# Kernel optimization log

Hardware: AMD Instinct MI355X
Metric: run time of the kernel (lower is better)

The kernel has to match this reference:

```python
import jax, jax.numpy as jnp
import numpy as np

N_NODES = 6890
N_ANGLES = 8
K_CHEB = 15
N_DESC = 544
HIDDEN = 64
N_CLASS = 6890
M = N_ANGLES * N_NODES  # 55120, size of anisotropic Laplacian
DEG = 16
NNZ = M * DEG
BN_EPS = 1e-5


def setup_inputs() -> dict:
    key = jax.random.key(0)
    ks = jax.random.split(key, 16)
    x = jax.random.normal(ks[0], (N_NODES, N_DESC), dtype=jnp.float32)
    # sparse anisotropic Laplacian (M x M), ~DEG nnz per row
    rows = jnp.repeat(jnp.arange(M, dtype=jnp.int32), DEG)
    cols = jax.random.randint(ks[1], (NNZ,), 0, M, dtype=jnp.int32)
    vals = jax.random.normal(ks[2], (NNZ,), dtype=jnp.float32) * 0.1
    # conv1: (K, n_angles*n_desc, 64); conv2..6 stacked: (5, K, n_angles*64, 64)
    def xavier(k, shape, fan_in, fan_out):
        lim = np.sqrt(6.0 / (fan_in + fan_out))
        return jax.random.uniform(k, shape, jnp.float32, -lim, lim)
    W1 = xavier(ks[3], (K_CHEB, N_ANGLES * N_DESC, HIDDEN), N_ANGLES * N_DESC, HIDDEN)
    Wc = xavier(ks[4], (5, K_CHEB, N_ANGLES * HIDDEN, HIDDEN), N_ANGLES * HIDDEN, HIDDEN)
    conv_b = jnp.zeros((6, HIDDEN), jnp.float32)
    bn_gamma = jnp.ones((6, HIDDEN), jnp.float32)
    bn_beta = jnp.zeros((6, HIDDEN), jnp.float32)
    fc2_w = xavier(ks[5], (HIDDEN, 256), HIDDEN, 256)
    fc2_b = jnp.zeros((256,), jnp.float32)
    fc3_w = xavier(ks[6], (256, N_CLASS), 256, N_CLASS)
    fc3_b = jnp.zeros((N_CLASS,), jnp.float32)
    return {"x": x, "rows": rows, "cols": cols, "vals": vals,
            "W1": W1, "Wc": Wc, "conv_b": conv_b,
            "bn_gamma": bn_gamma, "bn_beta": bn_beta,
            "fc2_w": fc2_w, "fc2_b": fc2_b, "fc3_w": fc3_w, "fc3_b": fc3_b}


def _spmm(rows, cols, vals, T):
    # (M x M sparse) @ (M x C) via gather + segment-sum
    return jax.ops.segment_sum(vals[:, None] * T[cols], rows, num_segments=M)


def _acs_conv(x, rows, cols, vals, W, b):
    # x: (N, C). Chebyshev recurrence on the (A*N, C) angle-stacked signal.
    N, C = x.shape
    A = N_ANGLES

    def proj(T, Wk):
        # (A*N, C) -> (N, A*C) @ (A*C, out)
        return T.reshape(A, N, C).transpose(1, 0, 2).reshape(N, A * C) @ Wk

    T0 = jnp.tile(x, (A, 1))
    out = proj(T0, W[0])
    T1 = _spmm(rows, cols, vals, T0)
    out = out + proj(T1, W[1])
    for k in range(2, K_CHEB):
        T2 = 2.0 * _spmm(rows, cols, vals, T1) - T0
        out = out + proj(T2, W[k])
        T0, T1 = T1, T2
    return out + b


def _bn_relu(x, gamma, beta):
    # BatchNorm1d (training-mode batch stats, biased variance) + ReLU
    mean = jnp.mean(x, axis=0)
    var = jnp.var(x, axis=0)
    return jax.nn.relu((x - mean) * jax.lax.rsqrt(var + BN_EPS) * gamma + beta)


def reference(x, rows, cols, vals, W1, Wc, conv_b, bn_gamma, bn_beta,
              fc2_w, fc2_b, fc3_w, fc3_b):
    h = _bn_relu(_acs_conv(x, rows, cols, vals, W1, conv_b[0]), bn_gamma[0], bn_beta[0])
    for i in range(5):
        h = _bn_relu(_acs_conv(h, rows, cols, vals, Wc[i], conv_b[i + 1]),
                     bn_gamma[i + 1], bn_beta[i + 1])
    h = jax.nn.relu(h @ fc2_w + fc2_b)
    # dropout is identity at inference
    return h @ fc3_w + fc3_b
```

## Files before the change

### kernel.cpp

```cpp
#include <hip/hip_runtime.h>
#include <cstdint>
#include <cstddef>

#define NN 6890
#define NA 8
#define KC 15
#define ND 544
#define MR (NA * NN)
#define DEG 16
#define NNZ (MR * DEG)
#define BN_EPS 1e-5f
#define NRG 108
#define PB (NA * NRG)

typedef unsigned int u32;
typedef _Float16 f16;
typedef __attribute__((ext_vector_type(8))) _Float16 f16x8;
typedef __attribute__((ext_vector_type(4))) float f32x4;

union U4H8 { uint4 q; f16 h[8]; f16x8 v; };

__device__ __forceinline__ u32 packh(float a, float b) {
    union { f16 h[2]; u32 u; } c;
    c.h[0] = (f16)a; c.h[1] = (f16)b; return c.u;
}
__device__ __forceinline__ uint4 pack8h(const float* t) {
    uint4 m;
    m.x = packh(t[0], t[1]); m.y = packh(t[2], t[3]);
    m.z = packh(t[4], t[5]); m.w = packh(t[6], t[7]);
    return m;
}
__device__ __forceinline__ void acc8h(float* s, float v, uint4 g) {
    U4H8 c; c.q = g;
    #pragma unroll
    for (int i = 0; i < 8; ++i) s[i] += v * (float)c.h[i];
}

__global__ __launch_bounds__(256)
void prep_cv_kernel(const int* __restrict__ cols, const float* __restrict__ vals,
                    uint4* __restrict__ cvq)
{
    const int q = blockIdx.x * 256 + threadIdx.x;
    if (q >= NNZ / 4) return;
    const int4   c = ((const int4*)cols)[q];
    const float4 v = ((const float4*)vals)[q];
    uint4 o;
    o.x = ((u32)c.x & 0xffffu) | ((u32)c.y << 16);
    o.y = ((u32)c.z & 0xffffu) | ((u32)c.w << 16);
    o.z = packh(v.x, v.y);
    o.w = packh(v.z, v.w);
    cvq[q] = o;
}

template<int CC, bool BN>
__global__ __launch_bounds__(256)
void tile_slab_kernel(const float* __restrict__ X, int C_in, int c0,
                      uint4* __restrict__ slab0, const float* __restrict__ bnp)
{
    constexpr int LPR = CC / 8;
    constexpr int RPB = 256 / LPR;
    const int tid = threadIdx.x;
    const int j = tid % LPR, rloc = tid / LPR;
    const int r = blockIdx.x * RPB + rloc;
    if (r >= MR) return;
    const int n = r % NN;
    const float* xp = X + (size_t)n * C_in + c0 + 8 * j;
    const float4 t0 = *(const float4*)xp;
    const float4 t1 = *(const float4*)(xp + 4);
    float t[8] = { t0.x, t0.y, t0.z, t0.w, t1.x, t1.y, t1.z, t1.w };
    if (BN) {
        const int ch = c0 + 8 * j;
        #pragma unroll
        for (int i = 0; i < 8; ++i) {
            const float v = t[i] * bnp[ch + i] + bnp[64 + ch + i];
            t[i] = v > 0.f ? v : 0.f;
        }
    }
    slab0[(size_t)r * LPR + j] = pack8h(t);
}

template<int CC, bool CHEB>
__device__ __forceinline__
void spmm_body(const uint4* __restrict__ sp, const uint4* __restrict__ sc,
               uint4* __restrict__ sw, const uint4* __restrict__ cvq,
               uint4* cvl)
{
    constexpr int LPR = CC / 8;
    constexpr int RPB = 256 / LPR;
    const int tid = threadIdx.x;
    const int j = tid % LPR, rloc = tid / LPR;
    const int r0 = blockIdx.x * RPB;
    const int nrow = (MR - r0) < RPB ? (MR - r0) : RPB;
    for (int e = tid; e < nrow * 4; e += 256)
        cvl[e] = cvq[(size_t)r0 * 4 + e];
    __syncthreads();
    const int r = r0 + rloc;
    if (r >= MR) return;

    int c[16]; float v[16];
    #pragma unroll
    for (int q = 0; q < 4; ++q) {
        const uint4 cq = cvl[rloc * 4 + q];
        c[4 * q + 0] = cq.x & 0xffffu; c[4 * q + 1] = cq.x >> 16;
        c[4 * q + 2] = cq.y & 0xffffu; c[4 * q + 3] = cq.y >> 16;
        union { u32 u; f16 h[2]; } z, w_;
        z.u = cq.z; w_.u = cq.w;
        v[4 * q + 0] = (float)z.h[0]; v[4 * q + 1] = (float)z.h[1];
        v[4 * q + 2] = (float)w_.h[0]; v[4 * q + 3] = (float)w_.h[1];
    }
    float s[8] = {0.f, 0.f, 0.f, 0.f, 0.f, 0.f, 0.f, 0.f};
    #pragma unroll
    for (int d = 0; d < DEG; ++d)
        acc8h(s, v[d], sp[(size_t)c[d] * LPR + j]);
    float t[8];
    if (CHEB) {
        U4H8 p; p.q = sc[(size_t)r * LPR + j];
        #pragma unroll
        for (int i = 0; i < 8; ++i) t[i] = 2.f * s[i] - (float)p.h[i];
    } else {
        #pragma unroll
        for (int i = 0; i < 8; ++i) t[i] = s[i];
    }
    sw[(size_t)r * LPR + j] = pack8h(t);
}

template<int CC, bool CHEB>
__global__ __launch_bounds__(256)
void spmm_only_kernel(const uint4* __restrict__ sp, const uint4* __restrict__ sc,
                      uint4* __restrict__ sw, const uint4* __restrict__ cvq)
{
    constexpr int RPB = 256 / (CC / 8);
    __shared__ uint4 cvl[RPB * 4];
    spmm_body<CC, CHEB>(sp, sc, sw, cvq, cvl);
}

template<int SCC, int NPROJ, bool FIRSTP>
__device__ __forceinline__
void proj_body(int pb, const uint4* __restrict__ s0, const uint4* __restrict__ s1,
               const float* __restrict__ W, float* __restrict__ part,
               int C_in, int c0, int kbase, u32* WH, u32* WL)
{
    constexpr int LPRF   = SCC / 8;
    constexpr int SLICES = SCC >= 64 ? SCC / 64 : 1;
    constexpr int SCH    = SCC >= 64 ? 64 : SCC;
    constexpr int CCH    = SCH / 32;
    const int tid = threadIdx.x;
    const int l = tid & 63, w = tid >> 6;
    const int a = pb / NRG, rg = pb % NRG;
    const int rows0 = rg * 64;
    const int hi16 = l >> 4;

    const int arow = rows0 + w * 16 + (l & 15);
    const int arc  = arow < NN ? arow : NN - 1;
    const size_t abase = (size_t)(a * NN + arc) * LPRF;

    f32x4 acc[4];
    #pragma unroll
    for (int nt = 0; nt < 4; ++nt) {
        #pragma unroll
        for (int rr = 0; rr < 4; ++rr) {
            const int orow = rows0 + w * 16 + hi16 * 4 + rr;
            float vv = 0.f;
            if (!FIRSTP && orow < NN)
                vv = part[((size_t)a * NN + orow) * 64 + nt * 16 + (l & 15)];
            acc[nt][rr] = vv;
        }
    }

    #pragma unroll
    for (int p = 0; p < NPROJ; ++p) {
        const uint4* sl = (p == 0) ? s0 : s1;
        #pragma unroll
        for (int s = 0; s < SLICES; ++s) {
            const float* Wk = W + ((size_t)(kbase + p) * NA * C_in
                                   + (size_t)a * C_in + c0 + s * 64) * 64;
            if (p | s) __syncthreads();
            for (int e = tid; e < CCH * 1024; e += 256) {
                const int i2 = e & 3;
                const int ll = (e >> 2) & 63;
                const int nt = (e >> 8) & 3;
                const int h  = e >> 10;
                const int cc  = h * 32 + (ll >> 4) * 8 + 2 * i2;
                const int col = nt * 16 + (ll & 15);
                const float w0 = Wk[(size_t)cc * 64 + col];
                const float w1 = Wk[(size_t)(cc + 1) * 64 + col];
                const f16 h0 = (f16)w0, h1 = (f16)w1;
                union { f16 h[2]; u32 u; } ph, pl;
                ph.h[0] = h0; ph.h[1] = h1;
                pl.h[0] = (f16)(w0 - (float)h0); pl.h[1] = (f16)(w1 - (float)h1);
                WH[e] = ph.u; WL[e] = pl.u;
            }
            __syncthreads();
            #pragma unroll
            for (int h = 0; h < CCH; ++h) {
                U4H8 af; af.q = sl[abase + s * 8 + h * 4 + hi16];
                #pragma unroll
                for (int nt = 0; nt < 4; ++nt) {
                    const int be = ((h * 4 + nt) * 64 + l) * 4;
                    U4H8 bh, bl;
                    bh.q = *(const uint4*)&WH[be];
                    bl.q = *(const uint4*)&WL[be];
                    acc[nt] = __builtin_amdgcn_mfma_f32_16x16x32_f16(af.v, bh.v, acc[nt], 0, 0, 0);
                    acc[nt] = __builtin_amdgcn_mfma_f32_16x16x32_f16(af.v, bl.v, acc[nt], 0, 0, 0);
                }
            }
        }
    }

    #pragma unroll
    for (int nt = 0; nt < 4; ++nt) {
        #pragma unroll
        for (int rr = 0; rr < 4; ++rr) {
            const int orow = rows0 + w * 16 + hi16 * 4 + rr;
            if (orow < NN)
                part[((size_t)a * NN + orow) * 64 + nt * 16 + (l & 15)] = acc[nt][rr];
        }
    }
}

template<int CC, bool FIRSTP>
__global__ __launch_bounds__(256)
void step2_kernel(const uint4* __restrict__ sp, const uint4* __restrict__ sc,
                  uint4* __restrict__ sw, const uint4* __restrict__ cvq,
                  const float* __restrict__ W, float* __restrict__ part,
                  int C_in, int c0, int kbase, int NB)
{
    constexpr int RPB = 256 / (CC / 8);
    __shared__ uint4 cvl[RPB * 4];
    __shared__ u32 WH[2048];
    __shared__ u32 WL[2048];
    if ((int)blockIdx.x < NB)
        spmm_body<CC, true>(sp, sc, sw, cvq, cvl);
    else
        proj_body<CC, 2, FIRSTP>((int)blockIdx.x - NB, sc, sp, W, part, C_in, c0, kbase, WH, WL);
}

template<int CC>
__global__ __launch_bounds__(256)
void proj_final_kernel(const uint4* __restrict__ sl, const float* __restrict__ W,
                       float* __restrict__ part, int C_in, int c0, int kproj)
{
    __shared__ u32 WH[2048];
    __shared__ u32 WL[2048];
    proj_body<CC, 1, false>((int)blockIdx.x, sl, sl, W, part, C_in, c0, kproj, WH, WL);
}

__global__ void bn_reduce_kernel(const float* __restrict__ part, float* __restrict__ acc)
{
    const int e = blockIdx.x * blockDim.x + threadIdx.x;
    if (e >= NN * 64) return;
    float s = 0.f;
    #pragma unroll
    for (int a = 0; a < NA; ++a) s += part[(size_t)a * NN * 64 + e];
    acc[e] = s;
}

__global__ __launch_bounds__(256)
void bn_stats_kernel(const float* __restrict__ acc, const float* __restrict__ gamma,
                     const float* __restrict__ beta, float* __restrict__ bnp)
{
    const int h = blockIdx.x;
    float s = 0.f, sq = 0.f;
    for (int n = threadIdx.x; n < NN; n += 256) {
        const float v = acc[(size_t)n * 64 + h];
        s += v; sq += v * v;
    }
    __shared__ float ls[256], lq[256];
    ls[threadIdx.x] = s; lq[threadIdx.x] = sq;
    __syncthreads();
    for (int st = 128; st > 0; st >>= 1) {
        if (threadIdx.x < st) { ls[threadIdx.x] += ls[threadIdx.x + st]; lq[threadIdx.x] += lq[threadIdx.x + st]; }
        __syncthreads();
    }
    if (threadIdx.x == 0) {
        const float mean = ls[0] / (float)NN;
        const float var  = lq[0] / (float)NN - mean * mean;
        const float sc   = gamma[h] / sqrtf(var + BN_EPS);
        bnp[h]      = sc;
        bnp[64 + h] = beta[h] - mean * sc;
    }
}

__global__ void bn_apply_kernel(const float* __restrict__ acc, const float* __restrict__ bnp,
                                float* __restrict__ H)
{
    const int e = blockIdx.x * blockDim.x + threadIdx.x;
    if (e >= NN * 64) return;
    const int h = e & 63;
    const float v = acc[e] * bnp[h] + bnp[64 + h];
    H[e] = v > 0.f ? v : 0.f;
}

template<bool RELU>
__global__ __launch_bounds__(256)
void gemm_bias_kernel(const float* __restrict__ A, const float* __restrict__ B,
                      const float* __restrict__ bias, float* __restrict__ C,
                      int Mm, int Nn, int Kk)
{
    __shared__ float As[16][132];
    __shared__ float Bs[16][132];
    const int tx = threadIdx.x & 15, ty = threadIdx.x >> 4;
    const int m0 = blockIdx.y * 128, n0 = blockIdx.x * 128;
    const bool full = (m0 + 128 <= Mm) && (n0 + 128 <= Nn);
    float acc[8][8] = {};
    for (int k0 = 0; k0 < Kk; k0 += 16) {
        if (full) {
            #pragma unroll
            for (int e = threadIdx.x; e < 512; e += 256) {
                const int i = e >> 2, q = e & 3;
                const float4 a4 = *(const float4*)&A[(size_t)(m0 + i) * Kk + k0 + 4 * q];
                As[4 * q + 0][i] = a4.x; As[4 * q + 1][i] = a4.y;
                As[4 * q + 2][i] = a4.z; As[4 * q + 3][i] = a4.w;
            }
            #pragma unroll
            for (int e = threadIdx.x; e < 512; e += 256) {
                const int kk = e >> 5, q = e & 31;
                *(float4*)&Bs[kk][4 * q] = *(const float4*)&B[(size_t)(k0 + kk) * Nn + n0 + 4 * q];
            }
        } else {
            for (int e = threadIdx.x; e < 128 * 16; e += 256) {
                const int i = e >> 4, kk = e & 15;
                const int row = m0 + i;
                As[kk][i] = (row < Mm) ? A[(size_t)row * Kk + k0 + kk] : 0.f;
            }
            for (int e = threadIdx.x; e < 16 * 128; e += 256) {
                const int kk = e >> 7, jj = e & 127;
                const int col = n0 + jj;
                Bs[kk][jj] = (col < Nn) ? B[(size_t)(k0 + kk) * Nn + col] : 0.f;
            }
        }
        __syncthreads();
        #pragma unroll
        for (int kk = 0; kk < 16; ++kk) {
            float av[8], bv[8];
            *(float4*)&av[0] = *(const float4*)&As[kk][ty * 4];
            *(float4*)&av[4] = *(const float4*)&As[kk][64 + ty * 4];
            *(float4*)&bv[0] = *(const float4*)&Bs[kk][tx * 4];
            *(float4*)&bv[4] = *(const float4*)&Bs[kk][64 + tx * 4];
            #pragma unroll
            for (int i = 0; i < 8; ++i)
                #pragma unroll
                for (int jj = 0; jj < 8; ++jj)
                    acc[i][jj] += av[i] * bv[jj];
        }
        __syncthreads();
    }
    for (int i = 0; i < 8; ++i) {
        const int row = m0 + (i < 4 ? ty * 4 + i : 64 + ty * 4 + (i - 4));
        if (row >= Mm) continue;
        for (int jj = 0; jj < 8; ++jj) {
            const int col = n0 + (jj < 4 ? tx * 4 + jj : 64 + tx * 4 + (jj - 4));
            if (col >= Nn) continue;
            float v = acc[i][jj] + bias[col];
            if (RELU) v = fmaxf(v, 0.f);
            C[(size_t)row * Nn + col] = v;
        }
    }
}

__global__ __launch_bounds__(256)
void w3_split_kernel(const float* __restrict__ W, f16* __restrict__ Wh, f16* __restrict__ Wl)
{
    __shared__ float t[64][65];
    const int tid = threadIdx.x;
    const int n0 = blockIdx.x * 64, k0 = blockIdx.y * 64;
    for (int e = tid; e < 64 * 64; e += 256) {
        const int kk = e >> 6, nn = e & 63;
        const int gn = n0 + nn;
        t[kk][nn] = (gn < NN) ? W[(size_t)(k0 + kk) * NN + gn] : 0.f;
    }
    __syncthreads();
    for (int e = tid; e < 64 * 8; e += 256) {
        const int nn = e >> 3, c8 = e & 7;
        const int gn = n0 + nn;
        if (gn >= NN) continue;
        const size_t ob = ((size_t)((k0 >> 3) + c8) * NN + gn) * 8;
        f16 vh[8], vl[8];
        #pragma unroll
        for (int i = 0; i < 8; ++i) {
            const float w = t[c8 * 8 + i][nn];
            const f16 h = (f16)w;
            vh[i] = h; vl[i] = (f16)(w - (float)h);
        }
        *(uint4*)&Wh[ob] = *(const uint4*)vh;
        *(uint4*)&Wl[ob] = *(const uint4*)vl;
    }
}

__global__ __launch_bounds__(256)
void f2_split_kernel(const float* __restrict__ f2, f16* __restrict__ Ah, f16* __restrict__ Al)
{
    const int row = blockIdx.x * 256 + threadIdx.x;
    const int c = blockIdx.y;
    if (row >= NN) return;
    const float4 a0 = *(const float4*)&f2[(size_t)row * 256 + c * 8];
    const float4 a1 = *(const float4*)&f2[(size_t)row * 256 + c * 8 + 4];
    const float vv[8] = { a0.x, a0.y, a0.z, a0.w, a1.x, a1.y, a1.z, a1.w };
    f16 vh[8], vl[8];
    #pragma unroll
    for (int i = 0; i < 8; ++i) {
        const f16 h = (f16)vv[i];
        vh[i] = h; vl[i] = (f16)(vv[i] - (float)h);
    }
    const size_t ob = ((size_t)c * NN + row) * 8;
    *(uint4*)&Ah[ob] = *(const uint4*)vh;
    *(uint4*)&Al[ob] = *(const uint4*)vl;
}

__global__ __launch_bounds__(256)
void fc3_mfma_kernel(const f16* __restrict__ Ah, const f16* __restrict__ Al,
                     const f16* __restrict__ Bh, const f16* __restrict__ Bl,
                     const float* __restrict__ bias, float* __restrict__ C)
{
    const int tid = threadIdx.x, l = tid & 63, w = tid >> 6;
    const int wm = w >> 1, wn = w & 1, hi16 = l >> 4;
    const int m0 = blockIdx.y * 128, n0 = blockIdx.x * 128;

    size_t aoff[4], boff[4];
    #pragma unroll
    for (int mf = 0; mf < 4; ++mf) {
        int row = m0 + wm * 64 + mf * 16 + (l & 15);
        if (row > NN - 1) row = NN - 1;
        aoff[mf] = (size_t)row * 8;
    }
    #pragma unroll
    for (int nf = 0; nf < 4; ++nf) {
        int col = n0 + wn * 64 + nf * 16 + (l & 15);
        if (col > NN - 1) col = NN - 1;
        boff[nf] = (size_t)col * 8;
    }

    f32x4 acc[4][4];
    #pragma unroll
    for (int mf = 0; mf < 4; ++mf)
        #pragma unroll
        for (int nf = 0; nf < 4; ++nf)
            acc[mf][nf] = (f32x4){0.f, 0.f, 0.f, 0.f};

    for (int k0 = 0; k0 < 256; k0 += 32) {
        const size_t cb = (size_t)((k0 >> 3) + hi16) * NN * 8;
        f16x8 ah[4], al[4], bh[4], bl[4];
        #pragma unroll
        for (int mf = 0; mf < 4; ++mf) {
            ah[mf] = *(const f16x8*)(Ah + cb + aoff[mf]);
            al[mf] = *(const f16x8*)(Al + cb + aoff[mf]);
        }
        #pragma unroll
        for (int nf = 0; nf < 4; ++nf) {
            bh[nf] = *(const f16x8*)(Bh + cb + boff[nf]);
            bl[nf] = *(const f16x8*)(Bl + cb + boff[nf]);
        }
        #pragma unroll
        for (int mf = 0; mf < 4; ++mf)
            #pragma unroll
            for (int nf = 0; nf < 4; ++nf) {
                acc[mf][nf] = __builtin_amdgcn_mfma_f32_16x16x32_f16(ah[mf], bh[nf], acc[mf][nf], 0, 0, 0);
                acc[mf][nf] = __builtin_amdgcn_mfma_f32_16x16x32_f16(ah[mf], bl[nf], acc[mf][nf], 0, 0, 0);
                acc[mf][nf] = __builtin_amdgcn_mfma_f32_16x16x32_f16(al[mf], bh[nf], acc[mf][nf], 0, 0, 0);
            }
    }

    #pragma unroll
    for (int mf = 0; mf < 4; ++mf) {
        #pragma unroll
        for (int nf = 0; nf < 4; ++nf) {
            const int col = n0 + wn * 64 + nf * 16 + (l & 15);
            if (col >= NN) continue;
            const float bv = bias[col];
            #pragma unroll
            for (int rr = 0; rr < 4; ++rr) {
                const int row = m0 + wm * 64 + mf * 16 + hi16 * 4 + rr;
                if (row < NN)
                    C[(size_t)row * NN + col] = acc[mf][nf][rr] + bv;
            }
        }
    }
}

template<int CC, bool BN>
static void run_chunk(bool first, const float* X, int C_in, int c0,
                      const uint4* cvq, const float* W, const float* bnp,
                      uint4* slabs, float* part, hipStream_t stream)
{
    constexpr int RPB = 256 / (CC / 8);
    const int NB = (MR + RPB - 1) / RPB;
    const size_t SLOT = (size_t)MR * (CC / 8);
    uint4* sl[3] = { slabs, slabs + SLOT, slabs + 2 * SLOT };

    tile_slab_kernel<CC, BN><<<NB, 256, 0, stream>>>(X, C_in, c0, sl[0], bnp);
    spmm_only_kernel<CC, false><<<NB, 256, 0, stream>>>(sl[0], sl[0], sl[1], cvq);
    for (int k = 2; k < KC; ++k) {
        const int p = (k - 1) % 3, c = (k - 2) % 3, n = k % 3;
        if (k & 1) {
            spmm_only_kernel<CC, true><<<NB, 256, 0, stream>>>(sl[p], sl[c], sl[n], cvq);
        } else {
            if (first && k == 2)
                step2_kernel<CC, true ><<<NB + PB, 256, 0, stream>>>(
                    sl[p], sl[c], sl[n], cvq, W, part, C_in, c0, k - 2, NB);
            else
                step2_kernel<CC, false><<<NB + PB, 256, 0, stream>>>(
                    sl[p], sl[c], sl[n], cvq, W, part, C_in, c0, k - 2, NB);
        }
    }
    proj_final_kernel<CC><<<PB, 256, 0, stream>>>(sl[(KC - 1) % 3], W, part, C_in, c0, KC - 1);
}

extern "C" void kernel_launch(void* const* d_in, const int* in_sizes, int n_in,
                              void* d_out, int out_size, void* d_ws, size_t ws_size,
                              hipStream_t stream)
{
    (void)in_sizes; (void)n_in; (void)out_size; (void)ws_size;
    const float* x     = (const float*)d_in[0];
    const int*   cols  = (const int*)  d_in[2];
    const float* vals  = (const float*)d_in[3];
    const float* W1    = (const float*)d_in[4];
    const float* Wc    = (const float*)d_in[5];
    const float* gamma = (const float*)d_in[7];
    const float* beta  = (const float*)d_in[8];
    const float* fc2w  = (const float*)d_in[9];
    const float* fc2b  = (const float*)d_in[10];
    const float* fc3w  = (const float*)d_in[11];
    const float* fc3b  = (const float*)d_in[12];

    const size_t MT = (size_t)MR * 64;

    uint4* slabs = (uint4*)d_out;

    char* base = (char*)d_ws;
    size_t off = 0;
    uint4* cvq  = (uint4*)(base + off); off += (size_t)(NNZ / 4) * 16;
    float* part = (float*)(base + off); off += MT * 4;
    float* acc  = (float*)(base + off); off += (size_t)NN * 64 * 4;
    float* H    = (float*)(base + off); off += (size_t)NN * 64 * 4;
    float* f2   = (float*)(base + off); off += (size_t)NN * 256 * 4;
    f16* f2h    = (f16*)(base + off);   off += (size_t)NN * 256 * 2;
    f16* f2l    = (f16*)(base + off);   off += (size_t)NN * 256 * 2;
    f16* W3h    = (f16*)(base + off);   off += (size_t)NN * 256 * 2;
    f16* W3l    = (f16*)(base + off);   off += (size_t)NN * 256 * 2;
    float* bnp  = (float*)(base + off);

    prep_cv_kernel<<<(NNZ / 4 + 255) / 256, 256, 0, stream>>>(cols, vals, cvq);
    w3_split_kernel<<<dim3(108, 4), 256, 0, stream>>>(fc3w, W3h, W3l);

    for (int li = 0; li < 6; ++li) {
        const int C_in = (li == 0) ? ND : 64;
        const float* W = (li == 0) ? W1 : Wc + (size_t)(li - 1) * KC * (NA * 64) * 64;

        if (li == 0) {
            run_chunk<256, false>(true,  x, C_in, 0,   cvq, W, nullptr, slabs, part, stream);
            run_chunk<256, false>(false, x, C_in, 256, cvq, W, nullptr, slabs, part, stream);
            run_chunk<32,  false>(false, x, C_in, 512, cvq, W, nullptr, slabs, part, stream);
        } else {
            run_chunk<64, true>(true, acc, C_in, 0, cvq, W, bnp, slabs, part, stream);
        }

        bn_reduce_kernel<<<(NN * 64 + 255) / 256, 256, 0, stream>>>(part, acc);
        bn_stats_kernel<<<64, 256, 0, stream>>>(acc, gamma + li * 64, beta + li * 64, bnp);
        if (li == 5)
            bn_apply_kernel<<<(NN * 64 + 255) / 256, 256, 0, stream>>>(acc, bnp, H);
    }

    gemm_bias_kernel<true><<<dim3(2, 54), 256, 0, stream>>>(H, fc2w, fc2b, f2, NN, 256, 64);
    f2_split_kernel<<<dim3(27, 32), 256, 0, stream>>>(f2, f2h, f2l);
    fc3_mfma_kernel<<<dim3(54, 54), 256, 0, stream>>>(f2h, f2l, W3h, W3l, fc3b, (float*)d_out);
}
```

Before: 4.085 ms.

## Batch layer-0 chunks into joint launches, batch projections, fuse fc2 split, remap fc3 tiles

Layer 0 previously ran three chunk pipelines one after another. They now run in single combined launches for tiling, SpMM and SpMM+projection, with separate ring buffers so the chunks proceed together. Hidden layers use a 5-slot ring so each projection pass handles four Chebyshev terms at once, which cuts the read-modify-write traffic on the partial accumulator. fc2 now writes the f16 hi/lo split directly, removing a kernel and an fp32 buffer, and fc3 uses an XCD-aware tile remap for better L2 locality. In exchange it needs more workspace and more complex kernels.

New measurement: 3.876 ms. 5.1% less time.

```diff
diff --git a/kernel.cpp b/kernel.cpp
--- a/kernel.cpp
+++ b/kernel.cpp
@@ -12,13 +12,19 @@
 #define BN_EPS 1e-5f
 #define NRG 108
 #define PB (NA * NRG)
+#define NB256 6890
+#define NB32  862
+#define NB64  1723
 
 typedef unsigned int u32;
 typedef _Float16 f16;
 typedef __attribute__((ext_vector_type(8))) _Float16 f16x8;
+typedef __attribute__((ext_vector_type(4))) _Float16 f16x4;
 typedef __attribute__((ext_vector_type(4))) float f32x4;
 
 union U4H8 { uint4 q; f16 h[8]; f16x8 v; };
+
+struct Slabs4 { const uint4* s[4]; };
 
 __device__ __forceinline__ u32 packh(float a, float b) {
     union { f16 h[2]; u32 u; } c;
@@ -53,15 +59,15 @@
 }
 
 template<int CC, bool BN>
-__global__ __launch_bounds__(256)
-void tile_slab_kernel(const float* __restrict__ X, int C_in, int c0,
-                      uint4* __restrict__ slab0, const float* __restrict__ bnp)
+__device__ __forceinline__
+void tile_body(int bid, const float* __restrict__ X, int C_in, int c0,
+               uint4* __restrict__ slab0, const float* __restrict__ bnp)
 {
     constexpr int LPR = CC / 8;
     constexpr int RPB = 256 / LPR;
     const int tid = threadIdx.x;
     const int j = tid % LPR, rloc = tid / LPR;
-    const int r = blockIdx.x * RPB + rloc;
+    const int r = bid * RPB + rloc;
     if (r >= MR) return;
     const int n = r % NN;
     const float* xp = X + (size_t)n * C_in + c0 + 8 * j;
@@ -79,17 +85,34 @@
     slab0[(size_t)r * LPR + j] = pack8h(t);
 }
 
+__global__ __launch_bounds__(256)
+void tile_l0_kernel(const float* __restrict__ X,
+                    uint4* __restrict__ sA, uint4* __restrict__ sB,
+                    uint4* __restrict__ sT)
+{
+    const int bid = blockIdx.x;
+    if (bid < NB256)            tile_body<256, false>(bid, X, ND, 0, sA, nullptr);
+    else if (bid < 2 * NB256)   tile_body<256, false>(bid - NB256, X, ND, 256, sB, nullptr);
+    else                        tile_body<32,  false>(bid - 2 * NB256, X, ND, 512, sT, nullptr);
+}
+
+__global__ __launch_bounds__(256)
+void tile64_bn_kernel(const float* __restrict__ X, uint4* __restrict__ slab0,
+                      const float* __restrict__ bnp)
+{
+    tile_body<64, true>(blockIdx.x, X, 64, 0, slab0, bnp);
+}
+
 template<int CC, bool CHEB>
 __device__ __forceinline__
-void spmm_body(const uint4* __restrict__ sp, const uint4* __restrict__ sc,
-               uint4* __restrict__ sw, const uint4* __restrict__ cvq,
-               uint4* cvl)
+void spmm_body(int bid, const uint4* __restrict__ sp, const uint4* __restrict__ sc,
+               uint4* __restrict__ sw, const uint4* __restrict__ cvq, uint4* cvl)
 {
     constexpr int LPR = CC / 8;
     constexpr int RPB = 256 / LPR;
     const int tid = threadIdx.x;
     const int j = tid % LPR, rloc = tid / LPR;
-    const int r0 = blockIdx.x * RPB;
+    const int r0 = bid * RPB;
     const int nrow = (MR - r0) < RPB ? (MR - r0) : RPB;
     for (int e = tid; e < nrow * 4; e += 256)
         cvl[e] = cvq[(size_t)r0 * 4 + e];
@@ -124,39 +147,14 @@
     sw[(size_t)r * LPR + j] = pack8h(t);
 }
 
-template<int CC, bool CHEB>
-__global__ __launch_bounds__(256)
-void spmm_only_kernel(const uint4* __restrict__ sp, const uint4* __restrict__ sc,
-                      uint4* __restrict__ sw, const uint4* __restrict__ cvq)
-{
-    constexpr int RPB = 256 / (CC / 8);
-    __shared__ uint4 cvl[RPB * 4];
-    spmm_body<CC, CHEB>(sp, sc, sw, cvq, cvl);
-}
-
-template<int SCC, int NPROJ, bool FIRSTP>
+template<bool FIRSTP>
 __device__ __forceinline__
-void proj_body(int pb, const uint4* __restrict__ s0, const uint4* __restrict__ s1,
-               const float* __restrict__ W, float* __restrict__ part,
-               int C_in, int c0, int kbase, u32* WH, u32* WL)
-{
-    constexpr int LPRF   = SCC / 8;
-    constexpr int SLICES = SCC >= 64 ? SCC / 64 : 1;
-    constexpr int SCH    = SCC >= 64 ? 64 : SCC;
-    constexpr int CCH    = SCH / 32;
-    const int tid = threadIdx.x;
-    const int l = tid & 63, w = tid >> 6;
-    const int a = pb / NRG, rg = pb % NRG;
-    const int rows0 = rg * 64;
+void proj_ld(f32x4 (&acc)[4], const float* __restrict__ part, int a, int rows0,
+             int l, int w)
+{
     const int hi16 = l >> 4;
-
-    const int arow = rows0 + w * 16 + (l & 15);
-    const int arc  = arow < NN ? arow : NN - 1;
-    const size_t abase = (size_t)(a * NN + arc) * LPRF;
-
-    f32x4 acc[4];
-    #pragma unroll
-    for (int nt = 0; nt < 4; ++nt) {
+    #pragma unroll
+    for (int nt = 0; nt < 4; ++nt)
         #pragma unroll
         for (int rr = 0; rr < 4; ++rr) {
             const int orow = rows0 + w * 16 + hi16 * 4 + rr;
@@ -165,16 +163,48 @@
                 vv = part[((size_t)a * NN + orow) * 64 + nt * 16 + (l & 15)];
             acc[nt][rr] = vv;
         }
-    }
+}
+
+__device__ __forceinline__
+void proj_st(const f32x4 (&acc)[4], float* __restrict__ part, int a, int rows0,
+             int l, int w)
+{
+    const int hi16 = l >> 4;
+    #pragma unroll
+    for (int nt = 0; nt < 4; ++nt)
+        #pragma unroll
+        for (int rr = 0; rr < 4; ++rr) {
+            const int orow = rows0 + w * 16 + hi16 * 4 + rr;
+            if (orow < NN)
+                part[((size_t)a * NN + orow) * 64 + nt * 16 + (l & 15)] = acc[nt][rr];
+        }
+}
+
+template<int SCC, int NPROJ>
+__device__ __forceinline__
+void proj_accum(int a, int rows0, int l, int w, Slabs4 sl,
+                const float* __restrict__ W, int C_in, int c0, int kbase,
+                u32* WH, u32* WL, f32x4 (&acc)[4], bool presync)
+{
+    constexpr int LPRF   = SCC / 8;
+    constexpr int SLICES = SCC >= 64 ? SCC / 64 : 1;
+    constexpr int SCH    = SCC >= 64 ? 64 : SCC;
+    constexpr int CCH    = SCH / 32;
+    const int tid = threadIdx.x;
+    const int hi16 = l >> 4;
+    const int arow = rows0 + w * 16 + (l & 15);
+    const int arc  = arow < NN ? arow : NN - 1;
+    const size_t abase = (size_t)(a * NN + arc) * LPRF;
 
     #pragma unroll
     for (int p = 0; p < NPROJ; ++p) {
-        const uint4* sl = (p == 0) ? s0 : s1;
+        const uint4* slab = sl.s[p];
         #pragma unroll
         for (int s = 0; s < SLICES; ++s) {
             const float* Wk = W + ((size_t)(kbase + p) * NA * C_in
                                    + (size_t)a * C_in + c0 + s * 64) * 64;
             if (p | s) __syncthreads();
+            else if (presync) __syncthreads();
             for (int e = tid; e < CCH * 1024; e += 256) {
                 const int i2 = e & 3;
                 const int ll = (e >> 2) & 63;
@@ -193,7 +223,7 @@
             __syncthreads();
             #pragma unroll
             for (int h = 0; h < CCH; ++h) {
-                U4H8 af; af.q = sl[abase + s * 8 + h * 4 + hi16];
+                U4H8 af; af.q = slab[abase + s * 8 + h * 4 + hi16];
                 #pragma unroll
                 for (int nt = 0; nt < 4; ++nt) {
                     const int be = ((h * 4 + nt) * 64 + l) * 4;
@@ -206,43 +236,115 @@
             }
         }
     }
-
-    #pragma unroll
-    for (int nt = 0; nt < 4; ++nt) {
-        #pragma unroll
-        for (int rr = 0; rr < 4; ++rr) {
-            const int orow = rows0 + w * 16 + hi16 * 4 + rr;
-            if (orow < NN)
-                part[((size_t)a * NN + orow) * 64 + nt * 16 + (l & 15)] = acc[nt][rr];
-        }
-    }
-}
-
-template<int CC, bool FIRSTP>
-__global__ __launch_bounds__(256)
-void step2_kernel(const uint4* __restrict__ sp, const uint4* __restrict__ sc,
-                  uint4* __restrict__ sw, const uint4* __restrict__ cvq,
-                  const float* __restrict__ W, float* __restrict__ part,
-                  int C_in, int c0, int kbase, int NB)
-{
-    constexpr int RPB = 256 / (CC / 8);
-    __shared__ uint4 cvl[RPB * 4];
+}
+
+template<bool CHEB>
+__global__ __launch_bounds__(256)
+void spmm_l0_kernel(const uint4* __restrict__ sAp, const uint4* __restrict__ sAc, uint4* __restrict__ sAw,
+                    const uint4* __restrict__ sBp, const uint4* __restrict__ sBc, uint4* __restrict__ sBw,
+                    const uint4* __restrict__ sTp, const uint4* __restrict__ sTc, uint4* __restrict__ sTw,
+                    const uint4* __restrict__ cvq)
+{
+    __shared__ uint4 cvl[256];
+    const int bid = blockIdx.x;
+    if (bid < NB256)          spmm_body<256, CHEB>(bid, sAp, sAc, sAw, cvq, cvl);
+    else if (bid < 2 * NB256) spmm_body<256, CHEB>(bid - NB256, sBp, sBc, sBw, cvq, cvl);
+    else                      spmm_body<32,  CHEB>(bid - 2 * NB256, sTp, sTc, sTw, cvq, cvl);
+}
+
+template<bool FIRSTP>
+__global__ __launch_bounds__(256)
+void step_l0_proj_kernel(const uint4* __restrict__ sAp, const uint4* __restrict__ sAc, uint4* __restrict__ sAw,
+                         const uint4* __restrict__ sBp, const uint4* __restrict__ sBc, uint4* __restrict__ sBw,
+                         const uint4* __restrict__ sTp, const uint4* __restrict__ sTc, uint4* __restrict__ sTw,
+                         const uint4* __restrict__ cvq, const float* __restrict__ W,
+                         float* __restrict__ part, int kbase)
+{
+    __shared__ uint4 cvl[256];
     __shared__ u32 WH[2048];
     __shared__ u32 WL[2048];
-    if ((int)blockIdx.x < NB)
-        spmm_body<CC, true>(sp, sc, sw, cvq, cvl);
-    else
-        proj_body<CC, 2, FIRSTP>((int)blockIdx.x - NB, sc, sp, W, part, C_in, c0, kbase, WH, WL);
-}
-
-template<int CC>
-__global__ __launch_bounds__(256)
-void proj_final_kernel(const uint4* __restrict__ sl, const float* __restrict__ W,
-                       float* __restrict__ part, int C_in, int c0, int kproj)
+    const int bid = blockIdx.x;
+    if (bid < NB256)          { spmm_body<256, true>(bid, sAp, sAc, sAw, cvq, cvl); return; }
+    if (bid < 2 * NB256)      { spmm_body<256, true>(bid - NB256, sBp, sBc, sBw, cvq, cvl); return; }
+    if (bid < 2 * NB256 + NB32) { spmm_body<32, true>(bid - 2 * NB256, sTp, sTc, sTw, cvq, cvl); return; }
+    const int pb = bid - (2 * NB256 + NB32);
+    const int l = threadIdx.x & 63, w = threadIdx.x >> 6;
+    const int a = pb / NRG, rows0 = (pb % NRG) * 64;
+    f32x4 acc[4];
+    proj_ld<FIRSTP>(acc, part, a, rows0, l, w);
+    Slabs4 sa; sa.s[0] = sAc; sa.s[1] = sAp;
+    Slabs4 sb; sb.s[0] = sBc; sb.s[1] = sBp;
+    Slabs4 st; st.s[0] = sTc; st.s[1] = sTp;
+    proj_accum<256, 2>(a, rows0, l, w, sa, W, ND, 0,   kbase, WH, WL, acc, false);
+    proj_accum<256, 2>(a, rows0, l, w, sb, W, ND, 256, kbase, WH, WL, acc, true);
+    proj_accum<32,  2>(a, rows0, l, w, st, W, ND, 512, kbase, WH, WL, acc, true);
+    proj_st(acc, part, a, rows0, l, w);
+}
+
+__global__ __launch_bounds__(256)
+void proj_l0_final_kernel(const uint4* __restrict__ sA, const uint4* __restrict__ sB,
+                          const uint4* __restrict__ sT, const float* __restrict__ W,
+                          float* __restrict__ part, int kbase)
 {
     __shared__ u32 WH[2048];
     __shared__ u32 WL[2048];
-    proj_body<CC, 1, false>((int)blockIdx.x, sl, sl, W, part, C_in, c0, kproj, WH, WL);
+    const int pb = blockIdx.x;
+    const int l = threadIdx.x & 63, w = threadIdx.x >> 6;
+    const int a = pb / NRG, rows0 = (pb % NRG) * 64;
+    f32x4 acc[4];
+    proj_ld<false>(acc, part, a, rows0, l, w);
+    Slabs4 sa; sa.s[0] = sA;
+    Slabs4 sb; sb.s[0] = sB;
+    Slabs4 st; st.s[0] = sT;
+    proj_accum<256, 1>(a, rows0, l, w, sa, W, ND, 0,   kbase, WH, WL, acc, false);
+    proj_accum<256, 1>(a, rows0, l, w, sb, W, ND, 256, kbase, WH, WL, acc, true);
+    proj_accum<32,  1>(a, rows0, l, w, st, W, ND, 512, kbase, WH, WL, acc, true);
+    proj_st(acc, part, a, rows0, l, w);
+}
+
+template<bool CHEB>
+__global__ __launch_bounds__(256)
+void spmm64_kernel(const uint4* __restrict__ sp, const uint4* __restrict__ sc,
+                   uint4* __restrict__ sw, const uint4* __restrict__ cvq)
+{
+    __shared__ uint4 cvl[128];
+    spmm_body<64, CHEB>(blockIdx.x, sp, sc, sw, cvq, cvl);
+}
+
+template<bool FIRSTP>
+__global__ __launch_bounds__(256)
+void step64_proj4_kernel(const uint4* __restrict__ sp, const uint4* __restrict__ sc,
+                         uint4* __restrict__ sw, Slabs4 prj,
+                         const uint4* __restrict__ cvq, const float* __restrict__ W,
+                         float* __restrict__ part, int kbase)
+{
+    __shared__ uint4 cvl[128];
+    __shared__ u32 WH[2048];
+    __shared__ u32 WL[2048];
+    const int bid = blockIdx.x;
+    if (bid < NB64) { spmm_body<64, true>(bid, sp, sc, sw, cvq, cvl); return; }
+    const int pb = bid - NB64;
+    const int l = threadIdx.x & 63, w = threadIdx.x >> 6;
+    const int a = pb / NRG, rows0 = (pb % NRG) * 64;
+    f32x4 acc[4];
+    proj_ld<FIRSTP>(acc, part, a, rows0, l, w);
+    proj_accum<64, 4>(a, rows0, l, w, prj, W, 64, 0, kbase, WH, WL, acc, false);
+    proj_st(acc, part, a, rows0, l, w);
+}
+
+__global__ __launch_bounds__(256)
+void proj64_final_kernel(Slabs4 prj, const float* __restrict__ W,
+                         float* __restrict__ part, int kbase)
+{
+    __shared__ u32 WH[2048];
+    __shared__ u32 WL[2048];
+    const int pb = blockIdx.x;
+    const int l = threadIdx.x & 63, w = threadIdx.x >> 6;
+    const int a = pb / NRG, rows0 = (pb % NRG) * 64;
+    f32x4 acc[4];
+    proj_ld<false>(acc, part, a, rows0, l, w);
+    proj_accum<64, 3>(a, rows0, l, w, prj, W, 64, 0, kbase, WH, WL, acc, false);
+    proj_st(acc, part, a, rows0, l, w);
 }
 
 __global__ void bn_reduce_kernel(const float* __restrict__ part, float* __restrict__ acc)
@@ -291,17 +393,17 @@
     H[e] = v > 0.f ? v : 0.f;
 }
 
-template<bool RELU>
-__global__ __launch_bounds__(256)
-void gemm_bias_kernel(const float* __restrict__ A, const float* __restrict__ B,
-                      const float* __restrict__ bias, float* __restrict__ C,
-                      int Mm, int Nn, int Kk)
-{
+__global__ __launch_bounds__(256)
+void fc2_kernel(const float* __restrict__ A, const float* __restrict__ B,
+                const float* __restrict__ bias,
+                f16* __restrict__ Oh, f16* __restrict__ Ol)
+{
+    constexpr int Kk = 64, Nn = 256;
     __shared__ float As[16][132];
     __shared__ float Bs[16][132];
     const int tx = threadIdx.x & 15, ty = threadIdx.x >> 4;
     const int m0 = blockIdx.y * 128, n0 = blockIdx.x * 128;
-    const bool full = (m0 + 128 <= Mm) && (n0 + 128 <= Nn);
+    const bool full = (m0 + 128 <= NN);
     float acc[8][8] = {};
     for (int k0 = 0; k0 < Kk; k0 += 16) {
         if (full) {
@@ -312,22 +414,17 @@
                 As[4 * q + 0][i] = a4.x; As[4 * q + 1][i] = a4.y;
                 As[4 * q + 2][i] = a4.z; As[4 * q + 3][i] = a4.w;
             }
-            #pragma unroll
-            for (int e = threadIdx.x; e < 512; e += 256) {
-                const int kk = e >> 5, q = e & 31;
-                *(float4*)&Bs[kk][4 * q] = *(const float4*)&B[(size_t)(k0 + kk) * Nn + n0 + 4 * q];
-            }
         } else {
             for (int e = threadIdx.x; e < 128 * 16; e += 256) {
                 const int i = e >> 4, kk = e & 15;
                 const int row = m0 + i;
-                As[kk][i] = (row < Mm) ? A[(size_t)row * Kk + k0 + kk] : 0.f;
-            }
-            for (int e = threadIdx.x; e < 16 * 128; e += 256) {
-                const int kk = e >> 7, jj = e & 127;
-                const int col = n0 + jj;
-                Bs[kk][jj] = (col < Nn) ? B[(size_t)(k0 + kk) * Nn + col] : 0.f;
-            }
+                As[kk][i] = (row < NN) ? A[(size_t)row * Kk + k0 + kk] : 0.f;
+            }
+        }
+        #pragma unroll
+        for (int e = threadIdx.x; e < 512; e += 256) {
+            const int kk = e >> 5, q = e & 31;
+            *(float4*)&Bs[kk][4 * q] = *(const float4*)&B[(size_t)(k0 + kk) * Nn + n0 + 4 * q];
         }
         __syncthreads();
         #pragma unroll
@@ -345,15 +442,24 @@
         }
         __syncthreads();
     }
+    #pragma unroll
     for (int i = 0; i < 8; ++i) {
         const int row = m0 + (i < 4 ? ty * 4 + i : 64 + ty * 4 + (i - 4));
-        if (row >= Mm) continue;
-        for (int jj = 0; jj < 8; ++jj) {
-            const int col = n0 + (jj < 4 ? tx * 4 + jj : 64 + tx * 4 + (jj - 4));
-            if (col >= Nn) continue;
-            float v = acc[i][jj] + bias[col];
-            if (RELU) v = fmaxf(v, 0.f);
-            C[(size_t)row * Nn + col] = v;
+        if (row >= NN) continue;
+        #pragma unroll
+        for (int g = 0; g < 2; ++g) {
+            const int colg = n0 + (g ? 64 : 0) + tx * 4;
+            f16x4 vh, vl;
+            #pragma unroll
+            for (int jj = 0; jj < 4; ++jj) {
+                float v = acc[i][g * 4 + jj] + bias[colg + jj];
+                v = fmaxf(v, 0.f);
+                const f16 h = (f16)v;
+                vh[jj] = h; vl[jj] = (f16)(v - (float)h);
+            }
+            const size_t ob = ((size_t)(colg >> 3) * NN + row) * 8 + (colg & 7);
+            *(f16x4*)&Oh[ob] = vh;
+            *(f16x4*)&Ol[ob] = vl;
         }
     }
 }
@@ -388,33 +494,19 @@
 }
 
 __global__ __launch_bounds__(256)
-void f2_split_kernel(const float* __restrict__ f2, f16* __restrict__ Ah, f16* __restrict__ Al)
-{
-    const int row = blockIdx.x * 256 + threadIdx.x;
-    const int c = blockIdx.y;
-    if (row >= NN) return;
-    const float4 a0 = *(const float4*)&f2[(size_t)row * 256 + c * 8];
-    const float4 a1 = *(const float4*)&f2[(size_t)row * 256 + c * 8 + 4];
-    const float vv[8] = { a0.x, a0.y, a0.z, a0.w, a1.x, a1.y, a1.z, a1.w };
-    f16 vh[8], vl[8];
-    #pragma unroll
-    for (int i = 0; i < 8; ++i) {
-        const f16 h = (f16)vv[i];
-        vh[i] = h; vl[i] = (f16)(vv[i] - (float)h);
-    }
-    const size_t ob = ((size_t)c * NN + row) * 8;
-    *(uint4*)&Ah[ob] = *(const uint4*)vh;
-    *(uint4*)&Al[ob] = *(const uint4*)vl;
-}
-
-__global__ __launch_bounds__(256)
 void fc3_mfma_kernel(const f16* __restrict__ Ah, const f16* __restrict__ Al,
                      const f16* __restrict__ Bh, const f16* __restrict__ Bl,
                      const float* __restrict__ bias, float* __restrict__ C)
 {
+    const int o = blockIdx.x;
+    const int xcd = o & 7, jj0 = o >> 3;
+    const int wg = (xcd < 4 ? xcd * 365 : 4 * 365 + (xcd - 4) * 364) + jj0;
+    const int band = wg / 486, inb = wg % 486;
+    const int mt = inb / 9, nt = band * 9 + inb % 9;
+    const int m0 = mt * 128, n0 = nt * 128;
+
     const int tid = threadIdx.x, l = tid & 63, w = tid >> 6;
     const int wm = w >> 1, wn = w & 1, hi16 = l >> 4;
-    const int m0 = blockIdx.y * 128, n0 = blockIdx.x * 128;
 
     size_t aoff[4], boff[4];
     #pragma unroll
@@ -475,34 +567,6 @@
             }
         }
     }
-}
-
-template<int CC, bool BN>
-static void run_chunk(bool first, const float* X, int C_in, int c0,
-                      const uint4* cvq, const float* W, const float* bnp,
-                      uint4* slabs, float* part, hipStream_t stream)
-{
-    constexpr int RPB = 256 / (CC / 8);
-    const int NB = (MR + RPB - 1) / RPB;
-    const size_t SLOT = (size_t)MR * (CC / 8);
-    uint4* sl[3] = { slabs, slabs + SLOT, slabs + 2 * SLOT };
-
-    tile_slab_kernel<CC, BN><<<NB, 256, 0, stream>>>(X, C_in, c0, sl[0], bnp);
-    spmm_only_kernel<CC, false><<<NB, 256, 0, stream>>>(sl[0], sl[0], sl[1], cvq);
-    for (int k = 2; k < KC; ++k) {
-        const int p = (k - 1) % 3, c = (k - 2) % 3, n = k % 3;
-        if (k & 1) {
-            spmm_only_kernel<CC, true><<<NB, 256, 0, stream>>>(sl[p], sl[c], sl[n], cvq);
-        } else {
-            if (first && k == 2)
-                step2_kernel<CC, true ><<<NB + PB, 256, 0, stream>>>(
-                    sl[p], sl[c], sl[n], cvq, W, part, C_in, c0, k - 2, NB);
-            else
-                step2_kernel<CC, false><<<NB + PB, 256, 0, stream>>>(
-                    sl[p], sl[c], sl[n], cvq, W, part, C_in, c0, k - 2, NB);
-        }
-    }
-    proj_final_kernel<CC><<<PB, 256, 0, stream>>>(sl[(KC - 1) % 3], W, part, C_in, c0, KC - 1);
 }
 
 extern "C" void kernel_launch(void* const* d_in, const int* in_sizes, int n_in,
@@ -524,43 +588,85 @@
 
     const size_t MT = (size_t)MR * 64;
 
-    uint4* slabs = (uint4*)d_out;
+    const size_t SL256 = (size_t)MR * 32;
+    const size_t SL32  = (size_t)MR * 4;
+    uint4* ringA = (uint4*)d_out;
+    uint4* ringB = ringA + 3 * SL256;
+    uint4* ringT = ringB + 3 * SL256;
+    auto slA = [&](int k) { return ringA + (size_t)(k % 3) * SL256; };
+    auto slB = [&](int k) { return ringB + (size_t)(k % 3) * SL256; };
+    auto slT = [&](int k) { return ringT + (size_t)(k % 3) * SL32; };
 
     char* base = (char*)d_ws;
     size_t off = 0;
     uint4* cvq  = (uint4*)(base + off); off += (size_t)(NNZ / 4) * 16;
+    uint4* ring5 = (uint4*)(base + off); off += 5 * (size_t)MR * 8 * 16;
     float* part = (float*)(base + off); off += MT * 4;
     float* acc  = (float*)(base + off); off += (size_t)NN * 64 * 4;
     float* H    = (float*)(base + off); off += (size_t)NN * 64 * 4;
-    float* f2   = (float*)(base + off); off += (size_t)NN * 256 * 4;
     f16* f2h    = (f16*)(base + off);   off += (size_t)NN * 256 * 2;
     f16* f2l    = (f16*)(base + off);   off += (size_t)NN * 256 * 2;
     f16* W3h    = (f16*)(base + off);   off += (size_t)NN * 256 * 2;
     f16* W3l    = (f16*)(base + off);   off += (size_t)NN * 256 * 2;
     float* bnp  = (float*)(base + off);
+    const size_t SL64 = (size_t)MR * 8;
+    auto sl5 = [&](int k) { return ring5 + (size_t)(k % 5) * SL64; };
 
     prep_cv_kernel<<<(NNZ / 4 + 255) / 256, 256, 0, stream>>>(cols, vals, cvq);
     w3_split_kernel<<<dim3(108, 4), 256, 0, stream>>>(fc3w, W3h, W3l);
 
-    for (int li = 0; li < 6; ++li) {
-        const int C_in = (li == 0) ? ND : 64;
-        const float* W = (li == 0) ? W1 : Wc + (size_t)(li - 1) * KC * (NA * 64) * 64;
-
-        if (li == 0) {
-            run_chunk<256, false>(true,  x, C_in, 0,   cvq, W, nullptr, slabs, part, stream);
-            run_chunk<256, false>(false, x, C_in, 256, cvq, W, nullptr, slabs, part, stream);
-            run_chunk<32,  false>(false, x, C_in, 512, cvq, W, nullptr, slabs, part, stream);
-        } else {
-            run_chunk<64, true>(true, acc, C_in, 0, cvq, W, bnp, slabs, part, stream);
-        }
-
+    {
+        const float* W = W1;
+        tile_l0_kernel<<<2 * NB256 + NB32, 256, 0, stream>>>(x, slA(0), slB(0), slT(0));
+        spmm_l0_kernel<false><<<2 * NB256 + NB32, 256, 0, stream>>>(
+            slA(0), slA(0), slA(1), slB(0), slB(0), slB(1), slT(0), slT(0), slT(1), cvq);
+        for (int k = 2; k < KC; ++k) {
+            if (k & 1) {
+                spmm_l0_kernel<true><<<2 * NB256 + NB32, 256, 0, stream>>>(
+                    slA(k - 1), slA(k - 2), slA(k), slB(k - 1), slB(k - 2), slB(k),
+                    slT(k - 1), slT(k - 2), slT(k), cvq);
+            } else if (k == 2) {
+                step_l0_proj_kernel<true><<<2 * NB256 + NB32 + PB, 256, 0, stream>>>(
+                    slA(k - 1), slA(k - 2), slA(k), slB(k - 1), slB(k - 2), slB(k),
+                    slT(k - 1), slT(k - 2), slT(k), cvq, W, part, k - 2);
+            } else {
+                step_l0_proj_kernel<false><<<2 * NB256 + NB32 + PB, 256, 0, stream>>>(
+                    slA(k - 1), slA(k - 2), slA(k), slB(k - 1), slB(k - 2), slB(k),
+                    slT(k - 1), slT(k - 2), slT(k), cvq, W, part, k - 2);
+            }
+        }
+        proj_l0_final_kernel<<<PB, 256, 0, stream>>>(slA(14), slB(14), slT(14), W, part, 14);
+        bn_reduce_kernel<<<(NN * 64 + 255) / 256, 256, 0, stream>>>(part, acc);
+        bn_stats_kernel<<<64, 256, 0, stream>>>(acc, gamma, beta, bnp);
+    }
+
+    for (int li = 1; li < 6; ++li) {
+        const float* W = Wc + (size_t)(li - 1) * KC * (NA * 64) * 64;
+        tile64_bn_kernel<<<NB64, 256, 0, stream>>>(acc, sl5(0), bnp);
+        spmm64_kernel<false><<<NB64, 256, 0, stream>>>(sl5(0), sl5(0), sl5(1), cvq);
+        for (int k = 2; k < KC; ++k) {
+            if (k == 4 || k == 8 || k == 12) {
+                Slabs4 prj;
+                prj.s[0] = sl5(k - 4); prj.s[1] = sl5(k - 3);
+                prj.s[2] = sl5(k - 2); prj.s[3] = sl5(k - 1);
+                if (k == 4)
+                    step64_proj4_kernel<true ><<<NB64 + PB, 256, 0, stream>>>(
+                        sl5(k - 1), sl5(k - 2), sl5(k), prj, cvq, W, part, k - 4);
+                else
+                    step64_proj4_kernel<false><<<NB64 + PB, 256, 0, stream>>>(
+                        sl5(k - 1), sl5(k - 2), sl5(k), prj, cvq, W, part, k - 4);
+            } else {
+                spmm64_kernel<true><<<NB64, 256, 0, stream>>>(sl5(k - 1), sl5(k - 2), sl5(k), cvq);
+            }
+        }
+        Slabs4 prjf;
+        prjf.s[0] = sl5(12); prjf.s[1] = sl5(13); prjf.s[2] = sl5(14); prjf.s[3] = sl5(14);
+        proj64_final_kernel<<<PB, 256, 0, stream>>>(prjf, W, part, 12);
         bn_reduce_kernel<<<(NN * 64 + 255) / 256, 256, 0, stream>>>(part, acc);
         bn_stats_kernel<<<64, 256, 0, stream>>>(acc, gamma + li * 64, beta + li * 64, bnp);
-        if (li == 5)
-            bn_apply_kernel<<<(NN * 64 + 255) / 256, 256, 0, stream>>>(acc, bnp, H);
-    }
-
-    gemm_bias_kernel<true><<<dim3(2, 54), 256, 0, stream>>>(H, fc2w, fc2b, f2, NN, 256, 64);
-    f2_split_kernel<<<dim3(27, 32), 256, 0, stream>>>(f2, f2h, f2l);
-    fc3_mfma_kernel<<<dim3(54, 54), 256, 0, stream>>>(f2h, f2l, W3h, W3l, fc3b, (float*)d_out);
-}
+    }
+
+    bn_apply_kernel<<<(NN * 64 + 255) / 256, 256, 0, stream>>>(acc, bnp, H);
+    fc2_kernel<<<dim3(2, 54), 256, 0, stream>>>(H, fc2w, fc2b, f2h, f2l);
+    fc3_mfma_kernel<<<2916, 256, 0, stream>>>(f2h, f2l, W3h, W3l, fc3b, (float*)d_out);
+}
```
